# Kernel optimization log

Measured on AMD Instinct MI355X. Metric: run time of the kernel, lower is better.

The kernel has to match this reference:

```python
import jax, jax.numpy as jnp
import numpy as np

SINK_MAX = 128  # max materialized sink tokens (atten_sink counts are < 64)
NEG_INF = -1e30


def _gather_paged(kv, block_table, pos):
    """Gather tokens from a paged KV cache.
    kv: [num_blocks, block_size, 2, Hkv, D]; block_table: [B, max_blocks] int;
    pos: [B, L] token positions (assumed clipped to valid range).
    Returns [B, L, 2, Hkv, D]."""
    nb, bs = kv.shape[0], kv.shape[1]
    B = pos.shape[0]
    blk = jnp.take_along_axis(block_table, pos // bs, axis=1)  # [B, L]
    flat_idx = blk * bs + pos % bs                              # [B, L]
    kv_flat = kv.reshape(nb * bs, *kv.shape[2:])
    return kv_flat[flat_idx]


def setup_inputs() -> dict:
    key = jax.random.key(0)
    ks = jax.random.split(key, 6)
    B, H, Hkv, D = 32, 32, 4, 128
    NB, BS, NBC = 2048, 128, 512
    MAX_BLK, MAX_CBLK, NSEL = 64, 16, 256
    query = jax.random.normal(ks[0], (B, H, D), dtype=jnp.float32)
    ori_kv = jax.random.normal(ks[1], (NB, BS, 2, Hkv, D), dtype=jnp.float32)
    cmp_kv = jax.random.normal(ks[2], (NBC, BS, 2, Hkv, D), dtype=jnp.float32)
    ori_block_table = (jnp.arange(B * MAX_BLK) % NB).reshape(B, MAX_BLK).astype(jnp.int32)
    cmp_block_table = (jnp.arange(B * MAX_CBLK) % NBC).reshape(B, MAX_CBLK).astype(jnp.int32)
    atten_sink = jax.random.randint(ks[3], (B,), 1, 64, dtype=jnp.int32)
    seqused_kv = jax.random.randint(ks[4], (B,), 4096, 8192, dtype=jnp.int32)
    cmp_sparse_indices = jnp.sort(jax.random.randint(ks[5], (B, NSEL), 0, 1024, dtype=jnp.int32), axis=1)
    return {
        'query_npu': query,
        'q_act_seqs_npu': jnp.ones((B,), dtype=jnp.int32),
        'ori_kv_npu': ori_kv,
        'cmp_kv_npu': cmp_kv,
        'ori_block_table_npu': ori_block_table,
        'cmp_block_table_npu': cmp_block_table,
        'atten_sink_npu': atten_sink,
        'seqused_kv_npu': seqused_kv,
        'cmp_sparse_indices_npu': cmp_sparse_indices,
        'softmax_scale': float(1.0 / np.sqrt(D)),
        'win_size': 512,
        'cmp_ratio': 4,
    }


def reference(query_npu, q_act_seqs_npu, ori_kv_npu, cmp_kv_npu,
              ori_block_table_npu, cmp_block_table_npu, atten_sink_npu,
              seqused_kv_npu, cmp_sparse_indices_npu, softmax_scale,
              win_size, cmp_ratio):
    B, H, D = query_npu.shape
    Hkv = ori_kv_npu.shape[3]
    G = H // Hkv
    bs = ori_kv_npu.shape[1]
    seq = seqused_kv_npu[:, None].astype(jnp.int32)          # [B,1]
    sink = atten_sink_npu[:, None].astype(jnp.int32)         # [B,1]

    # --- sink tokens (first atten_sink tokens of the original cache) ---
    pos_s = jnp.broadcast_to(jnp.arange(SINK_MAX, dtype=jnp.int32)[None, :], (B, SINK_MAX))
    mask_s = (pos_s < sink) & (pos_s < seq)
    kv_s = _gather_paged(ori_kv_npu, ori_block_table_npu, jnp.clip(pos_s, 0))

    # --- sliding window (last win_size original tokens, excluding sink overlap) ---
    pos_w = seq - win_size + jnp.arange(win_size, dtype=jnp.int32)[None, :]
    mask_w = (pos_w >= 0) & (pos_w >= sink)
    kv_w = _gather_paged(ori_kv_npu, ori_block_table_npu, jnp.clip(pos_w, 0))

    # --- sparse-selected compressed tokens ---
    cmp_len = seq // cmp_ratio
    idx_c = cmp_sparse_indices_npu.astype(jnp.int32)         # [B, NSEL]
    mask_c = idx_c < cmp_len
    kv_c = _gather_paged(cmp_kv_npu, cmp_block_table_npu, jnp.clip(idx_c, 0))

    # --- combine all KV sources: [B, L, 2, Hkv, D] ---
    kv = jnp.concatenate([kv_s, kv_w, kv_c], axis=1)
    k, v = kv[:, :, 0], kv[:, :, 1]                           # [B, L, Hkv, D]
    mask = jnp.concatenate([mask_s, mask_w, mask_c], axis=1)  # [B, L]

    # --- GQA attention: heads grouped per kv head ---
    q = query_npu.reshape(B, Hkv, G, D)
    logits = jnp.einsum('bkgd,blkd->bkgl', q, k) * softmax_scale
    logits = jnp.where(mask[:, None, None, :], logits, NEG_INF)
    p = jax.nn.softmax(logits, axis=-1)
    out = jnp.einsum('bkgl,blkd->bkgd', p, v)
    return out.reshape(B, H, D)
```

## Files before the change

kernel.cpp:

```cpp
#include <hip/hip_runtime.h>

constexpr int B_    = 32;
constexpr int H_    = 32;
constexpr int HKV_  = 4;
constexpr int G_    = 8;
constexpr int D_    = 128;
constexpr int BS_   = 128;
constexpr int MAXBLK_  = 64;
constexpr int MAXCBLK_ = 16;
constexpr int NSEL_    = 256;
constexpr int SINKMAX_ = 128;
constexpr int WIN_     = 512;
constexpr int P_       = 8;
constexpr float MSHIFT = 24.0f;

__global__ __launch_bounds__(256, 4) void sfa_partial_kernel(
    const float* __restrict__ q,
    const float* __restrict__ ori_kv,
    const float* __restrict__ cmp_kv,
    const int*   __restrict__ ori_bt,
    const int*   __restrict__ cmp_bt,
    const int*   __restrict__ sinkp,
    const int*   __restrict__ seqp,
    const int*   __restrict__ selp,
    const float* __restrict__ scalep,
    const int*   __restrict__ ratiop,
    float* __restrict__ o_out,
    float* __restrict__ s_out)
{
  const int part = blockIdx.x;
  const int kh   = blockIdx.y;
  const int b    = blockIdx.z;
  const int tid  = threadIdx.x;
  const int grp  = tid >> 5;
  const int j    = tid & 31;
  const int wave = tid >> 6;
  const int h    = ((j & 1) << 2) | (j & 2) | ((j >> 2) & 1);

  const float scale = scalep[0];
  const int ratio   = ratiop[0];
  const int seq     = seqp[b];
  const int sink    = sinkp[b];
  const int cmp_len = seq / ratio;

  const int sbt0 = ori_bt[b * MAXBLK_];
  int wbase = seq - WIN_; if (wbase < 0) wbase = 0;
  const int w0 = wbase >> 7;
  auto obt = [&](int k) { int w = w0 + k; if (w > MAXBLK_ - 1) w = MAXBLK_ - 1;
                          return ori_bt[b * MAXBLK_ + w]; };
  const int wb0 = obt(0), wb1 = obt(1), wb2 = obt(2), wb3 = obt(3), wb4 = obt(4);
  const int cb0 = cmp_bt[b * MAXCBLK_ + 0], cb1 = cmp_bt[b * MAXCBLK_ + 1];
  const int cb2 = cmp_bt[b * MAXCBLK_ + 2], cb3 = cmp_bt[b * MAXCBLK_ + 3];
  const int cb4 = cmp_bt[b * MAXCBLK_ + 4], cb5 = cmp_bt[b * MAXCBLK_ + 5];
  const int cb6 = cmp_bt[b * MAXCBLK_ + 6], cb7 = cmp_bt[b * MAXCBLK_ + 7];

  float4 qf[G_];
  const float* qb = q + ((size_t)b * H_ + (size_t)kh * G_) * D_ + 4 * j;
#pragma unroll
  for (int g = 0; g < G_; ++g) qf[g] = *(const float4*)(qb + g * D_);

  float  s_acc = 0.f;
  float4 oacc[G_];
#pragma unroll
  for (int m = 0; m < G_; ++m) oacc[m] = make_float4(0.f, 0.f, 0.f, 0.f);

  int s_end = sink; if (s_end < 0) s_end = 0; if (s_end > SINKMAX_) s_end = SINKMAX_;
  const int sB0 = s_end;
  const int sC0 = s_end + WIN_;
  const int L   = s_end + WIN_ + NSEL_;
  const int chunk = (L + P_ - 1) / P_;
  const int lo = part * chunk;
  int hi = lo + chunk; if (hi > L) hi = L;

  auto process = [&](const float4 kf, const float4 vf, const float msk) {
    float lg[G_];
#pragma unroll
    for (int g = 0; g < G_; ++g)
      lg[g] = qf[g].x * kf.x + qf[g].y * kf.y + qf[g].z * kf.z + qf[g].w * kf.w;
    const bool p0 = j & 1, p1 = j & 2, p2 = j & 4;
    float s4[4];
#pragma unroll
    for (int i4 = 0; i4 < 4; ++i4) {
      const float keep = p0 ? lg[4 + i4] : lg[i4];
      const float send = p0 ? lg[i4]     : lg[4 + i4];
      s4[i4] = keep + __shfl_xor(send, 1, 64);
    }
    float s2[2];
#pragma unroll
    for (int i2 = 0; i2 < 2; ++i2) {
      const float keep = p1 ? s4[2 + i2] : s4[i2];
      const float send = p1 ? s4[i2]     : s4[2 + i2];
      s2[i2] = keep + __shfl_xor(send, 2, 64);
    }
    const float keep = p2 ? s2[1] : s2[0];
    const float send = p2 ? s2[0] : s2[1];
    float v1 = keep + __shfl_xor(send, 4, 64);
    v1 += __shfl_xor(v1, 8, 64);
    v1 += __shfl_xor(v1, 16, 64);
    const float e = __expf(fminf(fmaf(v1, scale, -MSHIFT), 80.f)) * msk;
    s_acc += e;
    const float g2a = e,   g2b = __shfl_xor(e, 4, 64);
    const float g4a = g2a, g4b = g2b;
    const float g4c = __shfl_xor(g2a, 2, 64), g4d = __shfl_xor(g2b, 2, 64);
    const float pm0 = g4a, pm1 = g4b, pm2 = g4c, pm3 = g4d;
    const float pm4 = __shfl_xor(g4a, 1, 64), pm5 = __shfl_xor(g4b, 1, 64);
    const float pm6 = __shfl_xor(g4c, 1, 64), pm7 = __shfl_xor(g4d, 1, 64);
    oacc[0].x += pm0 * vf.x; oacc[0].y += pm0 * vf.y; oacc[0].z += pm0 * vf.z; oacc[0].w += pm0 * vf.w;
    oacc[1].x += pm1 * vf.x; oacc[1].y += pm1 * vf.y; oacc[1].z += pm1 * vf.z; oacc[1].w += pm1 * vf.w;
    oacc[2].x += pm2 * vf.x; oacc[2].y += pm2 * vf.y; oacc[2].z += pm2 * vf.z; oacc[2].w += pm2 * vf.w;
    oacc[3].x += pm3 * vf.x; oacc[3].y += pm3 * vf.y; oacc[3].z += pm3 * vf.z; oacc[3].w += pm3 * vf.w;
    oacc[4].x += pm4 * vf.x; oacc[4].y += pm4 * vf.y; oacc[4].z += pm4 * vf.z; oacc[4].w += pm4 * vf.w;
    oacc[5].x += pm5 * vf.x; oacc[5].y += pm5 * vf.y; oacc[5].z += pm5 * vf.z; oacc[5].w += pm5 * vf.w;
    oacc[6].x += pm6 * vf.x; oacc[6].y += pm6 * vf.y; oacc[6].z += pm6 * vf.z; oacc[6].w += pm6 * vf.w;
    oacc[7].x += pm7 * vf.x; oacc[7].y += pm7 * vf.y; oacc[7].z += pm7 * vf.z; oacc[7].w += pm7 * vf.w;
  };

#define SEG_LOOP(S0X, S1X, ADDR_CODE)                                          \
  {                                                                            \
    const int s0q = (S0X), s1q = (S1X);                                        \
    int iq = s0q + ((lo + grp - s0q) & 7);                                     \
    if (iq < s1q) {                                                            \
      const float* kbC; float mC;                                              \
      { const int ti = iq; const float* akb; float amsk; ADDR_CODE;            \
        kbC = akb; mC = amsk; }                                                \
      float4 kfC = *(const float4*)(kbC + 4 * j);                              \
      float4 vfC = *(const float4*)(kbC + HKV_ * D_ + 4 * j);                  \
      for (; iq < s1q; iq += 8) {                                              \
        int inq = iq + 8; if (inq >= s1q) inq = s1q - 1;                       \
        const float* kbN; float mN;                                            \
        { const int ti = inq; const float* akb; float amsk; ADDR_CODE;         \
          kbN = akb; mN = amsk; }                                              \
        const float4 kfN = *(const float4*)(kbN + 4 * j);                      \
        const float4 vfN = *(const float4*)(kbN + HKV_ * D_ + 4 * j);          \
        process(kfC, vfC, mC);                                                 \
        kfC = kfN; vfC = vfN; mC = mN;                                         \
      }                                                                        \
    }                                                                          \
  }

  SEG_LOOP(lo, (hi < sB0 ? hi : sB0), {
    amsk = (ti < seq) ? 1.f : 0.f;
    akb = ori_kv + (((size_t)(sbt0 * BS_ + ti)) << 10) + kh * D_;
  });

  SEG_LOOP((lo > sB0 ? lo : sB0), (hi < sC0 ? hi : sC0), {
    const int pos = seq - WIN_ + (ti - sB0);
    amsk = (pos >= 0 && pos >= sink) ? 1.f : 0.f;
    const int pc = pos > 0 ? pos : 0;
    const int wi = (pc >> 7) - w0;
    int blk = wb0;
    blk = (wi == 1) ? wb1 : blk; blk = (wi == 2) ? wb2 : blk;
    blk = (wi == 3) ? wb3 : blk; blk = (wi == 4) ? wb4 : blk;
    akb = ori_kv + (((size_t)(blk * BS_ + (pc & (BS_ - 1)))) << 10) + kh * D_;
  });

  SEG_LOOP((lo > sC0 ? lo : sC0), hi, {
    const int idx = selp[b * NSEL_ + (ti - sC0)];
    amsk = (idx < cmp_len) ? 1.f : 0.f;
    const int pc = idx > 0 ? idx : 0;
    const int ci = pc >> 7;
    int blk = cb0;
    blk = (ci == 1) ? cb1 : blk; blk = (ci == 2) ? cb2 : blk;
    blk = (ci == 3) ? cb3 : blk; blk = (ci == 4) ? cb4 : blk;
    blk = (ci == 5) ? cb5 : blk; blk = (ci == 6) ? cb6 : blk;
    blk = (ci == 7) ? cb7 : blk;
    akb = cmp_kv + (((size_t)(blk * BS_ + (pc & (BS_ - 1)))) << 10) + kh * D_;
  });
#undef SEG_LOOP

  s_acc += __shfl_xor(s_acc, 32, 64);
  float* of = reinterpret_cast<float*>(oacc);
#pragma unroll
  for (int t = 0; t < 32; ++t) of[t] += __shfl_xor(of[t], 32, 64);

  __shared__ float lds_o[4][G_][D_];
  __shared__ float lds_s[4][G_];
  if ((tid & 63) < 32) {
#pragma unroll
    for (int m = 0; m < G_; ++m)
      *(float4*)&lds_o[wave][h ^ m][4 * j] = oacc[m];
    if (j < 8) lds_s[wave][h] = s_acc;
  }
  __syncthreads();

#pragma unroll
  for (int e = tid; e < G_ * D_; e += 256) {
    const int g = e >> 7, d = e & (D_ - 1);
    const float num = lds_o[0][g][d] + lds_o[1][g][d] + lds_o[2][g][d] + lds_o[3][g][d];
    o_out[(((size_t)(b * HKV_ + kh) * P_ + part) * G_ + g) * D_ + d] = num;
  }
  if (tid < G_) {
    s_out[((size_t)(b * HKV_ + kh) * P_ + part) * G_ + tid] =
        lds_s[0][tid] + lds_s[1][tid] + lds_s[2][tid] + lds_s[3][tid];
  }
}

__global__ __launch_bounds__(256) void sfa_combine_kernel(
    const float* __restrict__ op, const float* __restrict__ sp,
    float* __restrict__ out)
{
  const int idx = blockIdx.x * 256 + threadIdx.x;
  const int d  = idx & (D_ - 1);
  const int hh = (idx >> 7) & (H_ - 1);
  const int b  = idx >> 12;
  const int kh = hh >> 3, g = hh & 7;
  float num = 0.f, den = 0.f;
#pragma unroll
  for (int p = 0; p < P_; ++p) {
    num += op[(((size_t)(b * HKV_ + kh) * P_ + p) * G_ + g) * D_ + d];
    den += sp[((size_t)(b * HKV_ + kh) * P_ + p) * G_ + g];
  }
  out[idx] = num / den;
}

extern "C" void kernel_launch(void* const* d_in, const int* in_sizes, int n_in,
                              void* d_out, int out_size, void* d_ws, size_t ws_size,
                              hipStream_t stream) {
  const float* q      = (const float*)d_in[0];
  const float* ori_kv = (const float*)d_in[2];
  const float* cmp_kv = (const float*)d_in[3];
  const int*   ori_bt = (const int*)d_in[4];
  const int*   cmp_bt = (const int*)d_in[5];
  const int*   sinkp  = (const int*)d_in[6];
  const int*   seqp   = (const int*)d_in[7];
  const int*   selp   = (const int*)d_in[8];
  const float* scalep = (const float*)d_in[9];
  const int*   ratiop = (const int*)d_in[11];
  float* out = (float*)d_out;

  float* op = (float*)d_ws;
  float* sp = op + (size_t)P_ * B_ * HKV_ * G_ * D_;

  sfa_partial_kernel<<<dim3(P_, HKV_, B_), 256, 0, stream>>>(
      q, ori_kv, cmp_kv, ori_bt, cmp_bt, sinkp, seqp, selp, scalep, ratiop,
      op, sp);
  sfa_combine_kernel<<<(B_ * H_ * D_) / 256, 256, 0, stream>>>(op, sp, out);
}
```

Baseline: 27.63 us.

## Replace wave shuffles with DPP/swizzle and preload sparse indices via lane shuffle

Swaps the ds_bpermute-based __shfl_xor reductions and broadcasts in the inner attention step for DPP row moves and ds_swizzle adds. It remaps the head-reduction butterfly to use lane xor 8 in place of xor 4 so that DPP can be used, and updates the head-index mapping and the LDS writer mask to match. It also loads each group's sparse indices once into a register per lane and fetches them with a shuffle instead of a global load per token. The aim is lower cross-lane latency and fewer dependent global loads, at the cost of subtle lane-mapping correctness risks.

```diff
diff --git a/kernel.cpp b/kernel.cpp
--- a/kernel.cpp
+++ b/kernel.cpp
@@ -13,6 +13,20 @@
 constexpr int WIN_     = 512;
 constexpr int P_       = 8;
 constexpr float MSHIFT = 24.0f;
+
+template <int CTRL>
+__device__ __forceinline__ float dpp_mov(float x) {
+  return __int_as_float(__builtin_amdgcn_update_dpp(
+      0, __float_as_int(x), CTRL, 0xF, 0xF, true));
+}
+constexpr int DPP_XOR1 = 0xB1;
+constexpr int DPP_XOR2 = 0x4E;
+constexpr int DPP_XOR8 = 0x128;
+template <int PATT>
+__device__ __forceinline__ float swz_add(float x) {
+  return x + __int_as_float(
+      __builtin_amdgcn_ds_swizzle(__float_as_int(x), PATT));
+}
 
 __global__ __launch_bounds__(256, 4) void sfa_partial_kernel(
     const float* __restrict__ q,
@@ -35,7 +49,9 @@
   const int grp  = tid >> 5;
   const int j    = tid & 31;
   const int wave = tid >> 6;
-  const int h    = ((j & 1) << 2) | (j & 2) | ((j >> 2) & 1);
+  const int lane = tid & 63;
+  const int h    = ((j & 1) << 2) | (j & 2) | ((j >> 3) & 1);
+  const bool wr8 = ((j & 20) == 0);
 
   const float scale = scalep[0];
   const int ratio   = ratiop[0];
@@ -71,41 +87,44 @@
   const int chunk = (L + P_ - 1) / P_;
   const int lo = part * chunk;
   int hi = lo + chunk; if (hi > L) hi = L;
+  const int cf = sC0 + (((lo + grp) - sC0) & 7);
+  const int sel_l = selp[b * NSEL_ + (cf - sC0) + 8 * j];
 
   auto process = [&](const float4 kf, const float4 vf, const float msk) {
     float lg[G_];
 #pragma unroll
     for (int g = 0; g < G_; ++g)
       lg[g] = qf[g].x * kf.x + qf[g].y * kf.y + qf[g].z * kf.z + qf[g].w * kf.w;
-    const bool p0 = j & 1, p1 = j & 2, p2 = j & 4;
+    const bool p0 = j & 1, p1 = j & 2, p3 = j & 8;
     float s4[4];
 #pragma unroll
     for (int i4 = 0; i4 < 4; ++i4) {
       const float keep = p0 ? lg[4 + i4] : lg[i4];
       const float send = p0 ? lg[i4]     : lg[4 + i4];
-      s4[i4] = keep + __shfl_xor(send, 1, 64);
+      s4[i4] = keep + dpp_mov<DPP_XOR1>(send);
     }
     float s2[2];
 #pragma unroll
     for (int i2 = 0; i2 < 2; ++i2) {
       const float keep = p1 ? s4[2 + i2] : s4[i2];
       const float send = p1 ? s4[i2]     : s4[2 + i2];
-      s2[i2] = keep + __shfl_xor(send, 2, 64);
+      s2[i2] = keep + dpp_mov<DPP_XOR2>(send);
     }
-    const float keep = p2 ? s2[1] : s2[0];
-    const float send = p2 ? s2[0] : s2[1];
-    float v1 = keep + __shfl_xor(send, 4, 64);
-    v1 += __shfl_xor(v1, 8, 64);
-    v1 += __shfl_xor(v1, 16, 64);
+    const float keep = p3 ? s2[1] : s2[0];
+    const float send = p3 ? s2[0] : s2[1];
+    float v1 = keep + dpp_mov<DPP_XOR8>(send);
+    v1 = swz_add<0x101F>(v1);
+    v1 = swz_add<0x401F>(v1);
     const float e = __expf(fminf(fmaf(v1, scale, -MSHIFT), 80.f)) * msk;
     s_acc += e;
-    const float g2a = e,   g2b = __shfl_xor(e, 4, 64);
-    const float g4a = g2a, g4b = g2b;
-    const float g4c = __shfl_xor(g2a, 2, 64), g4d = __shfl_xor(g2b, 2, 64);
-    const float pm0 = g4a, pm1 = g4b, pm2 = g4c, pm3 = g4d;
-    const float pm4 = __shfl_xor(g4a, 1, 64), pm5 = __shfl_xor(g4b, 1, 64);
-    const float pm6 = __shfl_xor(g4c, 1, 64), pm7 = __shfl_xor(g4d, 1, 64);
-    oacc[0].x += pm0 * vf.x; oacc[0].y += pm0 * vf.y; oacc[0].z += pm0 * vf.z; oacc[0].w += pm0 * vf.w;
+    const float pm1 = dpp_mov<DPP_XOR8>(e);
+    const float pm2 = dpp_mov<DPP_XOR2>(e);
+    const float pm3 = dpp_mov<DPP_XOR2>(pm1);
+    const float pm4 = dpp_mov<DPP_XOR1>(e);
+    const float pm5 = dpp_mov<DPP_XOR1>(pm1);
+    const float pm6 = dpp_mov<DPP_XOR1>(pm2);
+    const float pm7 = dpp_mov<DPP_XOR1>(pm3);
+    oacc[0].x += e   * vf.x; oacc[0].y += e   * vf.y; oacc[0].z += e   * vf.z; oacc[0].w += e   * vf.w;
     oacc[1].x += pm1 * vf.x; oacc[1].y += pm1 * vf.y; oacc[1].z += pm1 * vf.z; oacc[1].w += pm1 * vf.w;
     oacc[2].x += pm2 * vf.x; oacc[2].y += pm2 * vf.y; oacc[2].z += pm2 * vf.z; oacc[2].w += pm2 * vf.w;
     oacc[3].x += pm3 * vf.x; oacc[3].y += pm3 * vf.y; oacc[3].z += pm3 * vf.z; oacc[3].w += pm3 * vf.w;
@@ -155,7 +174,8 @@
   });
 
   SEG_LOOP((lo > sC0 ? lo : sC0), hi, {
-    const int idx = selp[b * NSEL_ + (ti - sC0)];
+    int mI = (ti - cf) >> 3; mI = mI < 0 ? 0 : (mI > 31 ? 31 : mI);
+    const int idx = __shfl(sel_l, mI, 32);
     amsk = (idx < cmp_len) ? 1.f : 0.f;
     const int pc = idx > 0 ? idx : 0;
     const int ci = pc >> 7;
@@ -175,11 +195,11 @@
 
   __shared__ float lds_o[4][G_][D_];
   __shared__ float lds_s[4][G_];
-  if ((tid & 63) < 32) {
+  if (lane < 32) {
 #pragma unroll
     for (int m = 0; m < G_; ++m)
       *(float4*)&lds_o[wave][h ^ m][4 * j] = oacc[m];
-    if (j < 8) lds_s[wave][h] = s_acc;
+    if (wr8) lds_s[wave][h] = s_acc;
   }
   __syncthreads();
 
```

Result: faster. 26.49 us (-4.1%).
